# Optimization experiments

Hardware: AMD Instinct MI355X
Metric: run time of the kernel (lower is better)

## Reference

```python
import jax, jax.numpy as jnp
import numpy as np

N = 100000   # num nodes
D = 128      # node_emb_dim
R = 8        # num_relations
E = 1600000  # num edges


def setup_inputs() -> dict:
    key = jax.random.key(0)
    k0, k1, k2, k3, k4 = jax.random.split(key, 5)
    x = jax.random.normal(k0, (N, D), dtype=jnp.float32)
    edge_index = jax.random.randint(k1, (2, E), 0, N, dtype=jnp.int32)
    edge_type = jax.random.randint(k2, (E,), 0, R, dtype=jnp.int32)
    scale = 1.0 / np.sqrt(D)
    W = (jax.random.normal(k3, (R, D, D), dtype=jnp.float32) * scale)       # per-relation weight
    W_root = (jax.random.normal(k4, (D, D), dtype=jnp.float32) * scale)     # root (self-loop) weight
    bias = jnp.zeros((D,), dtype=jnp.float32)
    return {"x": x, "W": W, "W_root": W_root, "bias": bias,
            "edge_index": edge_index, "edge_type": edge_type}


def reference(x, W, W_root, bias, edge_index, edge_type):
    # PyG RGCNConv (num_bases=None, aggr='mean', root_weight=True, bias=True):
    # out_i = x_i @ W_root + bias + sum_r mean_{j in N_r(i)} x_j @ W_r
    # Mean aggregation is linear, so aggregate neighbor features per (node, relation)
    # first, then apply the per-relation transform (avoids [E,D,D] intermediates).
    src, dst = edge_index[0], edge_index[1]
    seg = dst * R + edge_type                                   # [E] segment id per (dst, rel)
    cnt = jax.ops.segment_sum(jnp.ones((E,), x.dtype), seg, num_segments=N * R)  # [N*R]
    sums = jax.ops.segment_sum(x[src], seg, num_segments=N * R)                   # [N*R, D]
    mean = sums / jnp.maximum(cnt, 1.0)[:, None]                                  # [N*R, D]
    rel_out = jnp.einsum('nrd,rde->ne', mean.reshape(N, R, D), W)                 # [N, D]
    return rel_out + x @ W_root + bias
```

## Files before the change

kernel.cpp:

```cpp
#include <hip/hip_runtime.h>


constexpr int D = 128;
constexpr int R = 8;
constexpr int LDA = 40;
constexpr int TILE2 = 4096;
constexpr int CAP = 3072;
constexpr int MAXRUNS = 8192;
constexpr int TCH = 32;

typedef __bf16 bf16x8 __attribute__((ext_vector_type(8)));
typedef float  f32x4  __attribute__((ext_vector_type(4)));
typedef unsigned short u16x8 __attribute__((ext_vector_type(8)));
typedef unsigned short u16x4 __attribute__((ext_vector_type(4)));

__device__ __forceinline__ unsigned short f2bf(float f) {
    unsigned u = __builtin_bit_cast(unsigned, f);
    u += 0x7FFFu + ((u >> 16) & 1u);
    return (unsigned short)(u >> 16);
}
__device__ __forceinline__ float bf2f(unsigned short h) {
    return __builtin_bit_cast(float, (unsigned)h << 16);
}

__global__ __launch_bounds__(256)
void xbf_kernel(const float* __restrict__ x, unsigned short* __restrict__ xbf, int nquad) {
    int stride = gridDim.x * 256;
    for (int i = blockIdx.x * 256 + threadIdx.x; i < nquad; i += stride) {
        float4 v = ((const float4*)x)[i];
        u16x4 o;
        o[0] = f2bf(v.x); o[1] = f2bf(v.y); o[2] = f2bf(v.z); o[3] = f2bf(v.w);
        ((u16x4*)xbf)[i] = o;
    }
}

__global__ __launch_bounds__(256)
void count_kernel(const int* __restrict__ dst, const int* __restrict__ et,
                  unsigned short* __restrict__ counts, int E, int nruns) {
    __shared__ int lh[MAXRUNS];
    for (int i = threadIdx.x; i < nruns; i += 256) lh[i] = 0;
    __syncthreads();
    int t0 = blockIdx.x * TILE2;
    #pragma unroll 4
    for (int j = 0; j < TILE2 / 256; ++j) {
        int e = t0 + j * 256 + threadIdx.x;
        if (e < E) {
            int seg = dst[e] * R + et[e];
            atomicAdd(&lh[seg >> 7], 1);
        }
    }
    __syncthreads();
    unsigned short* row = counts + (size_t)blockIdx.x * nruns;
    for (int i = threadIdx.x; i < nruns; i += 256) row[i] = (unsigned short)lh[i];
}

__global__ __launch_bounds__(256)
void colscanA_kernel(const unsigned short* __restrict__ counts, int* __restrict__ part,
                     int ntiles, int nruns, int cpt) {
    int r = blockIdx.x * 256 + threadIdx.x;
    int c = blockIdx.y;
    if (r >= nruns) return;
    int t0 = c * cpt, t1 = min(t0 + cpt, ntiles);
    int acc = 0;
    for (int t = t0; t < t1; ++t) acc += counts[(size_t)t * nruns + r];
    part[(size_t)c * nruns + r] = acc;
}

__global__ __launch_bounds__(256)
void colscanB_kernel(int* __restrict__ part, int* __restrict__ runtot,
                     int nchunks, int nruns) {
    int r = blockIdx.x * 256 + threadIdx.x;
    if (r >= nruns) return;
    int acc = 0;
    for (int c = 0; c < nchunks; ++c) {
        size_t i = (size_t)c * nruns + r;
        int v = part[i];
        part[i] = acc;
        acc += v;
    }
    runtot[r] = acc;
}

__global__ __launch_bounds__(256)
void colscanC_kernel(unsigned short* __restrict__ counts, const int* __restrict__ part,
                     int ntiles, int nruns, int cpt) {
    int r = blockIdx.x * 256 + threadIdx.x;
    int c = blockIdx.y;
    if (r >= nruns) return;
    int t0 = c * cpt, t1 = min(t0 + cpt, ntiles);
    int acc = part[(size_t)c * nruns + r];
    for (int t = t0; t < t1; ++t) {
        size_t i = (size_t)t * nruns + r;
        int v = counts[i];
        counts[i] = (unsigned short)acc;
        acc += v;
    }
}

__global__ __launch_bounds__(64)
void runscan_kernel(const int* __restrict__ runtot, int* __restrict__ runbase, int nb) {
    int lane = threadIdx.x;
    int carry = 0;
    for (int base = 0; base < nb; base += 64) {
        int i = base + lane;
        int orig = (i < nb) ? runtot[i] : 0;
        int v = orig;
        #pragma unroll
        for (int off = 1; off < 64; off <<= 1) {
            int u = __shfl_up(v, off, 64);
            if (lane >= off) v += u;
        }
        int tot = __shfl(v, 63, 64);
        if (i < nb) runbase[i] = carry + (v - orig);
        carry += tot;
    }
    if (lane == 0) runbase[nb] = carry;
}

__global__ __launch_bounds__(256)
void place_kernel(const int* __restrict__ src, const int* __restrict__ dst,
                  const int* __restrict__ et, const unsigned short* __restrict__ counts,
                  const int* __restrict__ runbase, unsigned* __restrict__ epack,
                  int E, int nruns) {
    __shared__ int lh[MAXRUNS];
    for (int i = threadIdx.x; i < nruns; i += 256) lh[i] = 0;
    __syncthreads();
    int t0 = blockIdx.x * TILE2;
    const unsigned short* colpre = counts + (size_t)blockIdx.x * nruns;
    #pragma unroll 4
    for (int j = 0; j < TILE2 / 256; ++j) {
        int e = t0 + j * 256 + threadIdx.x;
        if (e < E) {
            int seg  = dst[e] * R + et[e];
            int run  = seg >> 7;
            int rank = atomicAdd(&lh[run], 1);
            int pos  = runbase[run] + (int)colpre[run] + rank;
            epack[pos] = (unsigned)src[e] | ((unsigned)(seg & 127) << 24);
        }
    }
}

template<int NOCT>
__global__ __launch_bounds__(256)
void aggregate_kernel(const unsigned short* __restrict__ xbf,
                      const unsigned* __restrict__ epack,
                      const int* __restrict__ runbase,
                      unsigned short* __restrict__ mean,
                      int nseg, int c0) {
    constexpr int GROUPS = 256 / NOCT;
    constexpr int SPT    = 128 / GROUPS;
    __shared__ unsigned raw[CAP];
    __shared__ unsigned srt[CAP];
    __shared__ int hist[128], sc[128], offs[128], cur[128];

    const int tid  = threadIdx.x;
    const int run  = blockIdx.x;
    const int base = runbase[run];
    const int size = runbase[run + 1] - base;
    const int c8   = tid & (NOCT - 1);
    const int sg0  = tid / NOCT;

    float a[SPT][8] = {};
    int   cacc[SPT] = {};

    const int nchunks = (size + CAP - 1) / CAP;
    for (int ch = 0; ch < nchunks; ++ch) {
        int off = ch * CAP;
        int n   = min(CAP, size - off);

        if (tid < 128) hist[tid] = 0;
        __syncthreads();
        for (int j = tid; j < n; j += 256) {
            unsigned e = epack[base + off + j];
            raw[j] = e;
            atomicAdd(&hist[e >> 24], 1);
        }
        __syncthreads();
        if (tid < 128) sc[tid] = hist[tid];
        __syncthreads();
        for (int o = 1; o < 128; o <<= 1) {
            int u = 0;
            if (tid < 128 && tid >= o) u = sc[tid - o];
            __syncthreads();
            if (tid < 128) sc[tid] += u;
            __syncthreads();
        }
        if (tid < 128) { int x0 = sc[tid] - hist[tid]; offs[tid] = x0; cur[tid] = x0; }
        __syncthreads();
        for (int j = tid; j < n; j += 256) {
            unsigned e = raw[j];
            int r = atomicAdd(&cur[e >> 24], 1);
            srt[r] = e;
        }
        __syncthreads();
        #pragma unroll
        for (int i = 0; i < SPT; ++i) {
            int s  = sg0 + i * GROUPS;
            int st = offs[s], cn = hist[s];
            cacc[i] += cn;
            for (int k = 0; k < cn; k += 4) {
                unsigned e0 = srt[st + k];
                int s1ok = (k + 1 < cn), s2ok = (k + 2 < cn), s3ok = (k + 3 < cn);
                unsigned e1 = s1ok ? srt[st + k + 1] : 0;
                unsigned e2 = s2ok ? srt[st + k + 2] : 0;
                unsigned e3 = s3ok ? srt[st + k + 3] : 0;
                u16x8 v0 = *(const u16x8*)(xbf + ((size_t)(e0 & 0xFFFFFF) << 7) + c0 + c8 * 8);
                #pragma unroll
                for (int q = 0; q < 8; ++q) a[i][q] += bf2f(v0[q]);
                if (s1ok) {
                    u16x8 v = *(const u16x8*)(xbf + ((size_t)(e1 & 0xFFFFFF) << 7) + c0 + c8 * 8);
                    #pragma unroll
                    for (int q = 0; q < 8; ++q) a[i][q] += bf2f(v[q]);
                }
                if (s2ok) {
                    u16x8 v = *(const u16x8*)(xbf + ((size_t)(e2 & 0xFFFFFF) << 7) + c0 + c8 * 8);
                    #pragma unroll
                    for (int q = 0; q < 8; ++q) a[i][q] += bf2f(v[q]);
                }
                if (s3ok) {
                    u16x8 v = *(const u16x8*)(xbf + ((size_t)(e3 & 0xFFFFFF) << 7) + c0 + c8 * 8);
                    #pragma unroll
                    for (int q = 0; q < 8; ++q) a[i][q] += bf2f(v[q]);
                }
            }
        }
        __syncthreads();
    }

    #pragma unroll
    for (int i = 0; i < SPT; ++i) {
        int seg = run * 128 + sg0 + i * GROUPS;
        if (seg < nseg) {
            float inv = (cacc[i] > 0) ? 1.0f / (float)cacc[i] : 0.0f;
            u16x8 o;
            #pragma unroll
            for (int q = 0; q < 8; ++q) o[q] = f2bf(a[i][q] * inv);
            __builtin_nontemporal_store(o,
                (u16x8*)(mean + (size_t)seg * (NOCT * 8) + c8 * 8));
        }
    }
}

__global__ __launch_bounds__(256)
void wallt_kernel(const float* __restrict__ Wroot, const float* __restrict__ W,
                  unsigned short* __restrict__ WallTc) {
    int idx = blockIdx.x * 256 + threadIdx.x;
    if (idx >= 128 * 1152) return;
    int n = idx / 1152, k = idx % 1152;
    float v = (k < 1024) ? W[(size_t)(k >> 7) * 16384 + (size_t)(k & 127) * 128 + n]
                         : Wroot[(size_t)(k - 1024) * 128 + n];
    WallTc[idx] = f2bf(v);
}

template<int MODE>
__global__ __launch_bounds__(256)
void mfma_gemm_kernel(const unsigned short* __restrict__ xbf,
                      const unsigned short* __restrict__ mean,
                      const unsigned short* __restrict__ WallTc,
                      const float* __restrict__ bias,
                      float* __restrict__ out,
                      int N, int c0) {
    constexpr int  NT      = (MODE == 0) ? 36 : (MODE == 1 ? 20 : 16);
    constexpr bool HASROOT = (MODE <= 1);
    __shared__ unsigned short As[64 * LDA];
    __shared__ unsigned short Bs[128 * LDA];
    const int tid  = threadIdx.x;
    const int nd0  = blockIdx.x * 64;
    const int lane = tid & 63;
    const int wid  = tid >> 6;
    const int wm   = wid >> 1;
    const int wn   = wid & 1;
    const int arow = tid >> 2;
    const int aoct = tid & 3;
    const int brow = tid >> 1;
    const int bhalf = tid & 1;

    f32x4 acc[2][4] = {};

    const int  anode = nd0 + arow;
    const bool aok   = anode < N;

    for (int kt = 0; kt < NT; ++kt) {
        if (kt) __syncthreads();
        u16x8 av8;
        #pragma unroll
        for (int j = 0; j < 8; ++j) av8[j] = 0;
        int kbase;
        if (HASROOT && kt < 4) {
            if (aok)
                av8 = *(const u16x8*)(xbf + ((size_t)anode << 7) + kt * 32 + aoct * 8);
            kbase = 1024 + kt * 32;
        } else {
            int lk = (kt - (HASROOT ? 4 : 0)) * 32;
            if (MODE == 0) {
                if (aok)
                    av8 = *(const u16x8*)(mean + ((size_t)anode << 10) + lk + aoct * 8);
                kbase = lk;
            } else {
                if (aok)
                    av8 = *(const u16x8*)(mean + ((size_t)anode << 9) + lk + aoct * 8);
                kbase = (lk >> 6) * 128 + c0 + (lk & 63);
            }
        }
        const u16x8* wp = (const u16x8*)(WallTc + (size_t)brow * 1152 + kbase + bhalf * 16);
        u16x8 b0 = wp[0], b1 = wp[1];

        *(u16x8*)&As[arow * LDA + aoct * 8]       = av8;
        *(u16x8*)&Bs[brow * LDA + bhalf * 16]     = b0;
        *(u16x8*)&Bs[brow * LDA + bhalf * 16 + 8] = b1;
        __syncthreads();

        const int ko = (lane >> 4) * 8;
        const int rl = lane & 15;
        bf16x8 af[2], bf[4];
        #pragma unroll
        for (int f = 0; f < 2; ++f)
            af[f] = __builtin_bit_cast(bf16x8,
                *(const u16x8*)&As[(wm * 32 + f * 16 + rl) * LDA + ko]);
        #pragma unroll
        for (int f = 0; f < 4; ++f)
            bf[f] = __builtin_bit_cast(bf16x8,
                *(const u16x8*)&Bs[(wn * 64 + f * 16 + rl) * LDA + ko]);
        #pragma unroll
        for (int mf = 0; mf < 2; ++mf)
            #pragma unroll
            for (int nf = 0; nf < 4; ++nf)
                acc[mf][nf] = __builtin_amdgcn_mfma_f32_16x16x32_bf16(af[mf], bf[nf],
                                                                     acc[mf][nf], 0, 0, 0);
    }

    const int rl = lane & 15;
    const int rg = lane >> 4;
    #pragma unroll
    for (int nf = 0; nf < 4; ++nf) {
        int n = wn * 64 + nf * 16 + rl;
        float bb = (MODE <= 1) ? bias[n] : 0.0f;
        #pragma unroll
        for (int mf = 0; mf < 2; ++mf) {
            #pragma unroll
            for (int i = 0; i < 4; ++i) {
                int nd = nd0 + wm * 32 + mf * 16 + rg * 4 + i;
                if (nd < N) {
                    size_t o = (size_t)nd * 128 + n;
                    if (MODE <= 1) out[o] = acc[mf][nf][i] + bb;
                    else           out[o] += acc[mf][nf][i];
                }
            }
        }
    }
}

extern "C" void kernel_launch(void* const* d_in, const int* in_sizes, int n_in,
                              void* d_out, int out_size, void* d_ws, size_t ws_size,
                              hipStream_t stream) {
    const float* x     = (const float*)d_in[0];
    const float* W     = (const float*)d_in[1];
    const float* Wroot = (const float*)d_in[2];
    const float* bias  = (const float*)d_in[3];
    const int*   ei    = (const int*)d_in[4];
    const int*   et    = (const int*)d_in[5];
    float*       out   = (float*)d_out;

    const int N = in_sizes[0] / D;
    const int E = in_sizes[5];
    const int* src = ei;
    const int* dst = ei + E;

    const int NSEG   = N * R;
    const int NRUNS  = (NSEG + 127) / 128;
    const int NTILES = (E + TILE2 - 1) / TILE2;
    if (NRUNS > MAXRUNS) return;

    const size_t xbf_bytes    = (size_t)N * D * 2;
    const size_t walltc_bytes = (size_t)128 * 1152 * 2;
    const size_t counts_bytes = (size_t)NTILES * NRUNS * 2;
    const size_t part_bytes   = (size_t)TCH * NRUNS * 4;
    const size_t tail_bytes   = counts_bytes + part_bytes +
                                ((size_t)NRUNS + (NRUNS + 1) + E) * 4 + 512;

    const size_t need128 = (size_t)NSEG * 128 * 2 + xbf_bytes + walltc_bytes + tail_bytes;
    const size_t need64  = (size_t)NSEG * 64  * 2 + xbf_bytes + walltc_bytes + tail_bytes;
    bool single = (need128 <= ws_size);
    if (!single && need64 > ws_size) return;

    const size_t mean_bytes = single ? (size_t)NSEG * 128 * 2 : (size_t)NSEG * 64 * 2;

    char* p = (char*)d_ws;
    unsigned short* mean   = (unsigned short*)p;  p += mean_bytes;
    unsigned short* xbf    = (unsigned short*)p;  p += xbf_bytes;
    unsigned short* WallTc = (unsigned short*)p;  p += walltc_bytes;
    unsigned short* counts = (unsigned short*)p;  p += counts_bytes;
    int*      part    = (int*)p;       p += part_bytes;
    int*      runtot  = (int*)p;       p += (size_t)NRUNS * 4;
    int*      runbase = (int*)p;       p += (size_t)(NRUNS + 1) * 4;
    unsigned* epack   = (unsigned*)p;

    xbf_kernel<<<1024, 256, 0, stream>>>(x, xbf, N * D / 4);
    wallt_kernel<<<(128 * 1152 + 255) / 256, 256, 0, stream>>>(Wroot, W, WallTc);

    count_kernel<<<NTILES, 256, 0, stream>>>(dst, et, counts, E, NRUNS);

    const int cpt = (NTILES + TCH - 1) / TCH;
    dim3 cgrid((NRUNS + 255) / 256, TCH);
    colscanA_kernel<<<cgrid, 256, 0, stream>>>(counts, part, NTILES, NRUNS, cpt);
    colscanB_kernel<<<(NRUNS + 255) / 256, 256, 0, stream>>>(part, runtot, TCH, NRUNS);
    colscanC_kernel<<<cgrid, 256, 0, stream>>>(counts, part, NTILES, NRUNS, cpt);
    runscan_kernel<<<1, 64, 0, stream>>>(runtot, runbase, NRUNS);

    place_kernel<<<NTILES, 256, 0, stream>>>(src, dst, et, counts, runbase, epack, E, NRUNS);

    const int gx = (N + 63) / 64;
    if (single) {
        aggregate_kernel<16><<<NRUNS, 256, 0, stream>>>(xbf, epack, runbase, mean, NSEG, 0);
        mfma_gemm_kernel<0><<<gx, 256, 0, stream>>>(xbf, mean, WallTc, bias, out, N, 0);
    } else {
        for (int c = 0; c < 2; ++c) {
            int c0 = c * 64;
            aggregate_kernel<8><<<NRUNS, 256, 0, stream>>>(xbf, epack, runbase, mean, NSEG, c0);
            if (c == 0)
                mfma_gemm_kernel<1><<<gx, 256, 0, stream>>>(xbf, mean, WallTc, bias, out, N, c0);
            else
                mfma_gemm_kernel<2><<<gx, 256, 0, stream>>>(xbf, mean, WallTc, bias, out, N, c0);
        }
    }
}
```

Baseline: 372.9 us.

## Fuse neighbor aggregation with relation GEMM via swizzled LDS means

Merges the aggregate and MFMA GEMM kernels into one kernel. Each run block (16 nodes × 8 relations) writes its bf16 means into an XOR-swizzled LDS tile, then multiplies them with the per-relation and root weights using MFMA and writes the output directly. This removes the global round trip of the N*R*D mean buffer and one kernel launch. In exchange each block reloads the full weight matrix from global/L2 and carries more register and LDS pressure. CAP is raised to 4096 so the chunk buffers fill the 32 KB pool that is reused for the means.

Measured after the change: 447.3 us. 1.2x slower.

```diff
diff --git a/kernel.cpp b/kernel.cpp
--- a/kernel.cpp
+++ b/kernel.cpp
@@ -3,9 +3,8 @@
 
 constexpr int D = 128;
 constexpr int R = 8;
-constexpr int LDA = 40;
 constexpr int TILE2 = 4096;
-constexpr int CAP = 3072;
+constexpr int CAP = 4096;
 constexpr int MAXRUNS = 8192;
 constexpr int TCH = 32;
 
@@ -140,28 +139,38 @@
     }
 }
 
-template<int NOCT>
-__global__ __launch_bounds__(256)
-void aggregate_kernel(const unsigned short* __restrict__ xbf,
-                      const unsigned* __restrict__ epack,
-                      const int* __restrict__ runbase,
-                      unsigned short* __restrict__ mean,
-                      int nseg, int c0) {
-    constexpr int GROUPS = 256 / NOCT;
-    constexpr int SPT    = 128 / GROUPS;
-    __shared__ unsigned raw[CAP];
-    __shared__ unsigned srt[CAP];
+__global__ __launch_bounds__(256)
+void wallt_kernel(const float* __restrict__ Wroot, const float* __restrict__ W,
+                  unsigned short* __restrict__ WallTc) {
+    int idx = blockIdx.x * 256 + threadIdx.x;
+    if (idx >= 128 * 1152) return;
+    int n = idx / 1152, k = idx % 1152;
+    float v = (k < 1024) ? W[(size_t)(k >> 7) * 16384 + (size_t)(k & 127) * 128 + n]
+                         : Wroot[(size_t)(k - 1024) * 128 + n];
+    WallTc[idx] = f2bf(v);
+}
+
+__global__ __launch_bounds__(256)
+void fused_kernel(const unsigned short* __restrict__ xbf,
+                  const unsigned short* __restrict__ WallTc,
+                  const unsigned* __restrict__ epack,
+                  const int* __restrict__ runbase,
+                  const float* __restrict__ bias,
+                  float* __restrict__ out, int N) {
+    __shared__ __align__(16) unsigned char pool[32768];
     __shared__ int hist[128], sc[128], offs[128], cur[128];
+    unsigned* raw = (unsigned*)pool;
+    unsigned* srt = (unsigned*)(pool + 16384);
 
     const int tid  = threadIdx.x;
     const int run  = blockIdx.x;
     const int base = runbase[run];
     const int size = runbase[run + 1] - base;
-    const int c8   = tid & (NOCT - 1);
-    const int sg0  = tid / NOCT;
-
-    float a[SPT][8] = {};
-    int   cacc[SPT] = {};
+    const int c8   = tid & 15;
+    const int sg0  = tid >> 4;
+
+    float a[8][8] = {};
+    int   cacc[8] = {};
 
     const int nchunks = (size + CAP - 1) / CAP;
     for (int ch = 0; ch < nchunks; ++ch) {
@@ -194,8 +203,8 @@
         }
         __syncthreads();
         #pragma unroll
-        for (int i = 0; i < SPT; ++i) {
-            int s  = sg0 + i * GROUPS;
+        for (int i = 0; i < 8; ++i) {
+            int s  = sg0 + i * 16;
             int st = offs[s], cn = hist[s];
             cacc[i] += cn;
             for (int k = 0; k < cn; k += 4) {
@@ -204,21 +213,21 @@
                 unsigned e1 = s1ok ? srt[st + k + 1] : 0;
                 unsigned e2 = s2ok ? srt[st + k + 2] : 0;
                 unsigned e3 = s3ok ? srt[st + k + 3] : 0;
-                u16x8 v0 = *(const u16x8*)(xbf + ((size_t)(e0 & 0xFFFFFF) << 7) + c0 + c8 * 8);
+                u16x8 v0 = *(const u16x8*)(xbf + ((size_t)(e0 & 0xFFFFFF) << 7) + c8 * 8);
                 #pragma unroll
                 for (int q = 0; q < 8; ++q) a[i][q] += bf2f(v0[q]);
                 if (s1ok) {
-                    u16x8 v = *(const u16x8*)(xbf + ((size_t)(e1 & 0xFFFFFF) << 7) + c0 + c8 * 8);
+                    u16x8 v = *(const u16x8*)(xbf + ((size_t)(e1 & 0xFFFFFF) << 7) + c8 * 8);
                     #pragma unroll
                     for (int q = 0; q < 8; ++q) a[i][q] += bf2f(v[q]);
                 }
                 if (s2ok) {
-                    u16x8 v = *(const u16x8*)(xbf + ((size_t)(e2 & 0xFFFFFF) << 7) + c0 + c8 * 8);
+                    u16x8 v = *(const u16x8*)(xbf + ((size_t)(e2 & 0xFFFFFF) << 7) + c8 * 8);
                     #pragma unroll
                     for (int q = 0; q < 8; ++q) a[i][q] += bf2f(v[q]);
                 }
                 if (s3ok) {
-                    u16x8 v = *(const u16x8*)(xbf + ((size_t)(e3 & 0xFFFFFF) << 7) + c0 + c8 * 8);
+                    u16x8 v = *(const u16x8*)(xbf + ((size_t)(e3 & 0xFFFFFF) << 7) + c8 * 8);
                     #pragma unroll
                     for (int q = 0; q < 8; ++q) a[i][q] += bf2f(v[q]);
                 }
@@ -228,124 +237,69 @@
     }
 
     #pragma unroll
-    for (int i = 0; i < SPT; ++i) {
-        int seg = run * 128 + sg0 + i * GROUPS;
-        if (seg < nseg) {
-            float inv = (cacc[i] > 0) ? 1.0f / (float)cacc[i] : 0.0f;
-            u16x8 o;
-            #pragma unroll
-            for (int q = 0; q < 8; ++q) o[q] = f2bf(a[i][q] * inv);
-            __builtin_nontemporal_store(o,
-                (u16x8*)(mean + (size_t)seg * (NOCT * 8) + c8 * 8));
-        }
-    }
-}
-
-__global__ __launch_bounds__(256)
-void wallt_kernel(const float* __restrict__ Wroot, const float* __restrict__ W,
-                  unsigned short* __restrict__ WallTc) {
-    int idx = blockIdx.x * 256 + threadIdx.x;
-    if (idx >= 128 * 1152) return;
-    int n = idx / 1152, k = idx % 1152;
-    float v = (k < 1024) ? W[(size_t)(k >> 7) * 16384 + (size_t)(k & 127) * 128 + n]
-                         : Wroot[(size_t)(k - 1024) * 128 + n];
-    WallTc[idx] = f2bf(v);
-}
-
-template<int MODE>
-__global__ __launch_bounds__(256)
-void mfma_gemm_kernel(const unsigned short* __restrict__ xbf,
-                      const unsigned short* __restrict__ mean,
-                      const unsigned short* __restrict__ WallTc,
-                      const float* __restrict__ bias,
-                      float* __restrict__ out,
-                      int N, int c0) {
-    constexpr int  NT      = (MODE == 0) ? 36 : (MODE == 1 ? 20 : 16);
-    constexpr bool HASROOT = (MODE <= 1);
-    __shared__ unsigned short As[64 * LDA];
-    __shared__ unsigned short Bs[128 * LDA];
-    const int tid  = threadIdx.x;
-    const int nd0  = blockIdx.x * 64;
+    for (int i = 0; i < 8; ++i) {
+        int ls = sg0 + i * 16;
+        float inv = (cacc[i] > 0) ? 1.0f / (float)cacc[i] : 0.0f;
+        u16x8 o;
+        #pragma unroll
+        for (int q = 0; q < 8; ++q) o[q] = f2bf(a[i][q] * inv);
+        *(u16x8*)(pool + ls * 256 + ((c8 * 16) ^ (((ls >> 3) & 15) << 4))) = o;
+    }
+    __syncthreads();
+
     const int lane = tid & 63;
     const int wid  = tid >> 6;
-    const int wm   = wid >> 1;
-    const int wn   = wid & 1;
-    const int arow = tid >> 2;
-    const int aoct = tid & 3;
-    const int brow = tid >> 1;
-    const int bhalf = tid & 1;
-
-    f32x4 acc[2][4] = {};
-
-    const int  anode = nd0 + arow;
-    const bool aok   = anode < N;
-
-    for (int kt = 0; kt < NT; ++kt) {
-        if (kt) __syncthreads();
-        u16x8 av8;
-        #pragma unroll
-        for (int j = 0; j < 8; ++j) av8[j] = 0;
-        int kbase;
-        if (HASROOT && kt < 4) {
-            if (aok)
-                av8 = *(const u16x8*)(xbf + ((size_t)anode << 7) + kt * 32 + aoct * 8);
-            kbase = 1024 + kt * 32;
-        } else {
-            int lk = (kt - (HASROOT ? 4 : 0)) * 32;
-            if (MODE == 0) {
-                if (aok)
-                    av8 = *(const u16x8*)(mean + ((size_t)anode << 10) + lk + aoct * 8);
-                kbase = lk;
-            } else {
-                if (aok)
-                    av8 = *(const u16x8*)(mean + ((size_t)anode << 9) + lk + aoct * 8);
-                kbase = (lk >> 6) * 128 + c0 + (lk & 63);
+    const int rl   = lane & 15;
+    const int rg   = lane >> 4;
+    const int kg16 = rg * 16;
+    const int nd0n = run * 16;
+
+    f32x4 oacc[2] = {};
+
+    #pragma unroll
+    for (int r = 0; r < 8; ++r) {
+        #pragma unroll
+        for (int kk = 0; kk < 4; ++kk) {
+            int lsr = rl * 8 + r;
+            bf16x8 av = __builtin_bit_cast(bf16x8,
+                *(const u16x8*)(pool + lsr * 256 + ((kk * 64 + kg16) ^ (rl << 4))));
+            #pragma unroll
+            for (int j = 0; j < 2; ++j) {
+                int nb = wid * 2 + j;
+                bf16x8 bv = __builtin_bit_cast(bf16x8,
+                    *(const u16x8*)(WallTc + (size_t)(nb * 16 + rl) * 1152
+                                    + r * 128 + kk * 32 + rg * 8));
+                oacc[j] = __builtin_amdgcn_mfma_f32_16x16x32_bf16(av, bv, oacc[j], 0, 0, 0);
             }
         }
-        const u16x8* wp = (const u16x8*)(WallTc + (size_t)brow * 1152 + kbase + bhalf * 16);
-        u16x8 b0 = wp[0], b1 = wp[1];
-
-        *(u16x8*)&As[arow * LDA + aoct * 8]       = av8;
-        *(u16x8*)&Bs[brow * LDA + bhalf * 16]     = b0;
-        *(u16x8*)&Bs[brow * LDA + bhalf * 16 + 8] = b1;
-        __syncthreads();
-
-        const int ko = (lane >> 4) * 8;
-        const int rl = lane & 15;
-        bf16x8 af[2], bf[4];
-        #pragma unroll
-        for (int f = 0; f < 2; ++f)
-            af[f] = __builtin_bit_cast(bf16x8,
-                *(const u16x8*)&As[(wm * 32 + f * 16 + rl) * LDA + ko]);
-        #pragma unroll
-        for (int f = 0; f < 4; ++f)
-            bf[f] = __builtin_bit_cast(bf16x8,
-                *(const u16x8*)&Bs[(wn * 64 + f * 16 + rl) * LDA + ko]);
-        #pragma unroll
-        for (int mf = 0; mf < 2; ++mf)
-            #pragma unroll
-            for (int nf = 0; nf < 4; ++nf)
-                acc[mf][nf] = __builtin_amdgcn_mfma_f32_16x16x32_bf16(af[mf], bf[nf],
-                                                                     acc[mf][nf], 0, 0, 0);
-    }
-
-    const int rl = lane & 15;
-    const int rg = lane >> 4;
+    }
     #pragma unroll
-    for (int nf = 0; nf < 4; ++nf) {
-        int n = wn * 64 + nf * 16 + rl;
-        float bb = (MODE <= 1) ? bias[n] : 0.0f;
-        #pragma unroll
-        for (int mf = 0; mf < 2; ++mf) {
-            #pragma unroll
-            for (int i = 0; i < 4; ++i) {
-                int nd = nd0 + wm * 32 + mf * 16 + rg * 4 + i;
-                if (nd < N) {
-                    size_t o = (size_t)nd * 128 + n;
-                    if (MODE <= 1) out[o] = acc[mf][nf][i] + bb;
-                    else           out[o] += acc[mf][nf][i];
-                }
-            }
+    for (int kt = 0; kt < 4; ++kt) {
+        int node = nd0n + rl;
+        u16x8 ax;
+        #pragma unroll
+        for (int q = 0; q < 8; ++q) ax[q] = 0;
+        if (node < N)
+            ax = *(const u16x8*)(xbf + ((size_t)node << 7) + kt * 32 + rg * 8);
+        bf16x8 av = __builtin_bit_cast(bf16x8, ax);
+        #pragma unroll
+        for (int j = 0; j < 2; ++j) {
+            int nb = wid * 2 + j;
+            bf16x8 bv = __builtin_bit_cast(bf16x8,
+                *(const u16x8*)(WallTc + (size_t)(nb * 16 + rl) * 1152
+                                + 1024 + kt * 32 + rg * 8));
+            oacc[j] = __builtin_amdgcn_mfma_f32_16x16x32_bf16(av, bv, oacc[j], 0, 0, 0);
+        }
+    }
+    #pragma unroll
+    for (int j = 0; j < 2; ++j) {
+        int nb  = wid * 2 + j;
+        int col = nb * 16 + rl;
+        float bb = bias[col];
+        #pragma unroll
+        for (int i2 = 0; i2 < 4; ++i2) {
+            int node = nd0n + rg * 4 + i2;
+            if (node < N) out[(size_t)node * 128 + col] = oacc[j][i2] + bb;
         }
     }
 }
@@ -375,18 +329,11 @@
     const size_t walltc_bytes = (size_t)128 * 1152 * 2;
     const size_t counts_bytes = (size_t)NTILES * NRUNS * 2;
     const size_t part_bytes   = (size_t)TCH * NRUNS * 4;
-    const size_t tail_bytes   = counts_bytes + part_bytes +
-                                ((size_t)NRUNS + (NRUNS + 1) + E) * 4 + 512;
-
-    const size_t need128 = (size_t)NSEG * 128 * 2 + xbf_bytes + walltc_bytes + tail_bytes;
-    const size_t need64  = (size_t)NSEG * 64  * 2 + xbf_bytes + walltc_bytes + tail_bytes;
-    bool single = (need128 <= ws_size);
-    if (!single && need64 > ws_size) return;
-
-    const size_t mean_bytes = single ? (size_t)NSEG * 128 * 2 : (size_t)NSEG * 64 * 2;
+    const size_t need = xbf_bytes + walltc_bytes + counts_bytes + part_bytes +
+                        ((size_t)NRUNS + (NRUNS + 1) + E) * 4 + 512;
+    if (ws_size < need) return;
 
     char* p = (char*)d_ws;
-    unsigned short* mean   = (unsigned short*)p;  p += mean_bytes;
     unsigned short* xbf    = (unsigned short*)p;  p += xbf_bytes;
     unsigned short* WallTc = (unsigned short*)p;  p += walltc_bytes;
     unsigned short* counts = (unsigned short*)p;  p += counts_bytes;
@@ -409,18 +356,5 @@
 
     place_kernel<<<NTILES, 256, 0, stream>>>(src, dst, et, counts, runbase, epack, E, NRUNS);
 
-    const int gx = (N + 63) / 64;
-    if (single) {
-        aggregate_kernel<16><<<NRUNS, 256, 0, stream>>>(xbf, epack, runbase, mean, NSEG, 0);
-        mfma_gemm_kernel<0><<<gx, 256, 0, stream>>>(xbf, mean, WallTc, bias, out, N, 0);
-    } else {
-        for (int c = 0; c < 2; ++c) {
-            int c0 = c * 64;
-            aggregate_kernel<8><<<NRUNS, 256, 0, stream>>>(xbf, epack, runbase, mean, NSEG, c0);
-            if (c == 0)
-                mfma_gemm_kernel<1><<<gx, 256, 0, stream>>>(xbf, mean, WallTc, bias, out, N, c0);
-            else
-                mfma_gemm_kernel<2><<<gx, 256, 0, stream>>>(xbf, mean, WallTc, bias, out, N, c0);
-        }
-    }
-}
+    fused_kernel<<<NRUNS, 256, 0, stream>>>(xbf, WallTc, epack, runbase, bias, out, N);
+}
```
